# Kernel optimization log

Hardware: AMD Instinct MI355X
Metric: run time of the kernel (lower is better)

The kernel has to match this reference:

```python
import jax, jax.numpy as jnp
import numpy as np

N_HEADS = 16

def setup_inputs() -> dict:
    key = jax.random.key(0)
    ks = jax.random.split(key, 8)
    B, S, D = 2, 2048, 1024
    s = 0.02
    return {
        "hidden_states": jax.random.normal(ks[0], (B, S, D), jnp.float32),
        "attention_mask": jnp.ones((B, S), jnp.int32),
        "script_types": jax.random.randint(ks[1], (B, S), 0, 4),
        "Wq": jax.random.normal(ks[2], (D, D), jnp.float32) * s,
        "bq": jnp.zeros((D,), jnp.float32),
        "Wk": jax.random.normal(ks[3], (D, D), jnp.float32) * s,
        "bk": jnp.zeros((D,), jnp.float32),
        "Wv": jax.random.normal(ks[4], (D, D), jnp.float32) * s,
        "bv": jnp.zeros((D,), jnp.float32),
        "Wo": jax.random.normal(ks[5], (D, D), jnp.float32) * s,
        "bo": jnp.zeros((D,), jnp.float32),
        "script_w": jnp.ones((4, N_HEADS), jnp.float32),
    }

def _heads(x, H):
    B, S, D = x.shape
    return x.reshape(B, S, H, D // H).transpose(0, 2, 1, 3)  # [B,H,S,hd]

def reference(hidden_states, attention_mask, script_types, Wq, bq, Wk, bk, Wv, bv, Wo, bo, script_w):
    B, S, D = hidden_states.shape
    H = N_HEADS
    hd = D // H
    q = _heads(hidden_states @ Wq + bq, H)
    k = _heads(hidden_states @ Wk + bk, H)
    v = _heads(hidden_states @ Wv + bv, H)
    # script-dependent per-head query scaling: [B,S,H] -> [B,H,S,1]
    sw = script_w[script_types].transpose(0, 2, 1)[..., None]
    q = q * sw
    scores = jnp.einsum("bhqd,bhkd->bhqk", q, k) / jnp.sqrt(jnp.float32(hd))
    mask = attention_mask[:, None, None, :]  # [B,1,1,S]
    scores = jnp.where(mask == 0, -jnp.inf, scores)
    probs = jax.nn.softmax(scores, axis=-1)  # dropout is identity in eval mode
    ctx = jnp.einsum("bhqk,bhkd->bhqd", probs, v)
    ctx = ctx.transpose(0, 2, 1, 3).reshape(B, S, D)
    out = ctx @ Wo + bo
    return out, probs
```

## Files before the change

### kernel.cpp

```cpp
#include <hip/hip_runtime.h>
#include <hip/hip_bf16.h>
#include <cstdint>
#include <cstddef>

typedef __attribute__((ext_vector_type(8))) short short8;
typedef __attribute__((ext_vector_type(4))) float f32x4;

#define MFMA16(a,b,c) __builtin_amdgcn_mfma_f32_16x16x32_bf16((a),(b),(c),0,0,0)
#define NEG_INF (-__builtin_inff())

__device__ __forceinline__ unsigned short f2bf(float f) {
    union { float f; unsigned int u; } a; a.f = f;
    return (unsigned short)((a.u + 0x7FFFu + ((a.u >> 16) & 1u)) >> 16);
}

__device__ __forceinline__ unsigned int cvtpk_bf16(float a, float b) {
    unsigned int r;
    asm("v_cvt_pk_bf16_f32 %0, %1, %2" : "=v"(r) : "v"(a), "v"(b));
    return r;
}

__device__ __forceinline__ void gload16(const void* g, void* l) {
    __builtin_amdgcn_global_load_lds(
        (const __attribute__((address_space(1))) void*)g,
        (__attribute__((address_space(3))) void*)l, 16, 0, 0);
}

__global__ __launch_bounds__(256) void prep(const float* __restrict__ X,
                                            unsigned short* __restrict__ Xb,
                                            const float* __restrict__ Wq,
                                            const float* __restrict__ Wk,
                                            const float* __restrict__ Wv,
                                            const float* __restrict__ Wo,
                                            unsigned short* __restrict__ WqkvT,
                                            unsigned short* __restrict__ WoT,
                                            const float* __restrict__ bq,
                                            const float* __restrict__ bk,
                                            const float* __restrict__ bv,
                                            float* __restrict__ biasq) {
    const int bid = blockIdx.x;
    const int t = threadIdx.x;
    if (bid < 4096) {
        int i = (bid * 256 + t) * 4;
        float4 v = *(const float4*)(X + i);
        ushort4 o;
        o.x = f2bf(v.x); o.y = f2bf(v.y); o.z = f2bf(v.z); o.w = f2bf(v.w);
        *(ushort4*)(Xb + i) = o;
    } else if (bid < 8192) {
        __shared__ float tile[32][33];
        const int wid = bid - 4096;
        const int which = wid >> 10, t32 = wid & 1023;
        const float* W = (which == 0) ? Wq : (which == 1) ? Wk : (which == 2) ? Wv : Wo;
        unsigned short* WT = (which < 3) ? (WqkvT + which * 1048576) : WoT;
        int tx = t & 31, ty = t >> 5;
        int kb = (t32 & 31) * 32, nb = (t32 >> 5) * 32;
        #pragma unroll
        for (int r = 0; r < 32; r += 8)
            tile[ty + r][tx] = W[(size_t)(kb + ty + r) * 1024 + nb + tx];
        __syncthreads();
        #pragma unroll
        for (int r = 0; r < 32; r += 8) {
            float v = tile[tx][ty + r];
            WT[(size_t)(nb + ty + r) * 1024 + kb + tx] = f2bf(v);
        }
    } else {
        for (int i = t; i < 3072; i += 256) {
            const float* s = (i < 1024) ? bq : (i < 2048) ? bk : bv;
            biasq[i] = s[i & 1023];
        }
    }
}

__global__ __launch_bounds__(256) void gemm_qkv(const unsigned short* __restrict__ A,
                                                const unsigned short* __restrict__ BT,
                                                const float* __restrict__ bias,
                                                unsigned short* __restrict__ qk_out,
                                                unsigned short* __restrict__ vt_out) {
    __shared__ alignas(16) unsigned short As[4096];
    __shared__ alignas(16) unsigned short Bs[4096];
    const int t = threadIdx.x;
    const int wave = t >> 6, lane = t & 63, quad = lane >> 4, l16 = lane & 15;
    const int m0 = blockIdx.x * 128, n0 = blockIdx.y * 128;
    const int wm = (wave >> 1) * 64, wn = (wave & 1) * 64;
    const int r4 = lane >> 2, c16 = (lane & 3) << 4;
    const char* Ag = (const char*)A + (size_t)(m0 + wave * 32 + r4) * 2048 + c16;
    const char* Bg = (const char*)BT + (size_t)(n0 + wave * 32 + r4) * 2048 + c16;
    char* Al = (char*)As + wave * 2048;
    char* Bl = (char*)Bs + wave * 2048;
    f32x4 acc[4][4] = {};
    for (int k0 = 0; k0 < 1024; k0 += 32) {
        __syncthreads();
        gload16(Ag + k0 * 2, Al);
        gload16(Ag + k0 * 2 + 32768, Al + 1024);
        gload16(Bg + k0 * 2, Bl);
        gload16(Bg + k0 * 2 + 32768, Bl + 1024);
        __syncthreads();
        short8 af[4], bfr[4];
        #pragma unroll
        for (int i = 0; i < 4; i++)
            af[i] = *(const short8*)((const char*)As + (wm + i * 16 + l16) * 64 + (quad << 4));
        #pragma unroll
        for (int j = 0; j < 4; j++)
            bfr[j] = *(const short8*)((const char*)Bs + (wn + j * 16 + l16) * 64 + (quad << 4));
        #pragma unroll
        for (int i = 0; i < 4; i++)
            #pragma unroll
            for (int j = 0; j < 4; j++)
                acc[i][j] = MFMA16(af[i], bfr[j], acc[i][j]);
    }
    #pragma unroll
    for (int i = 0; i < 4; i++) {
        int tokb = m0 + wm + i * 16 + quad * 4;
        int b = tokb >> 11, s = tokb & 2047;
        #pragma unroll
        for (int j = 0; j < 4; j++) {
            int n = n0 + wn + j * 16 + l16;
            float bv = bias[n];
            int which = n >> 10, n1 = n & 1023, h = n1 >> 6, d = n1 & 63;
            if (which == 2) {
                ushort4 pv;
                pv.x = f2bf(acc[i][j][0] + bv);
                pv.y = f2bf(acc[i][j][1] + bv);
                pv.z = f2bf(acc[i][j][2] + bv);
                pv.w = f2bf(acc[i][j][3] + bv);
                *(ushort4*)(vt_out + ((size_t)(b * 16 + h) * 64 + d) * 2048 + s) = pv;
            } else {
                #pragma unroll
                for (int r = 0; r < 4; r++) {
                    float v = acc[i][j][r] + bv;
                    qk_out[(size_t)which * 4194304 +
                           (((size_t)(b * 16 + h)) * 2048 + s + r) * 64 + d] = f2bf(v);
                }
            }
        }
    }
}

__global__ __launch_bounds__(256) void gemm_out(const unsigned short* __restrict__ A,
                                                const unsigned short* __restrict__ BT,
                                                const float* __restrict__ bias,
                                                float* __restrict__ C) {
    __shared__ alignas(16) unsigned short As[2048];
    __shared__ alignas(16) unsigned short Bs[4096];
    const int t = threadIdx.x;
    const int wave = t >> 6, lane = t & 63, quad = lane >> 4, l16 = lane & 15;
    const int m0 = blockIdx.x * 64, n0 = blockIdx.y * 128;
    const int wm = (wave >> 1) * 32, wn = (wave & 1) * 64;
    const int r4 = lane >> 2, c16 = (lane & 3) << 4;
    const char* Ag = (const char*)A + (size_t)(m0 + wave * 16 + r4) * 2048 + c16;
    const char* Bg = (const char*)BT + (size_t)(n0 + wave * 32 + r4) * 2048 + c16;
    char* Al = (char*)As + wave * 1024;
    char* Bl = (char*)Bs + wave * 2048;
    f32x4 acc[2][4] = {};
    for (int k0 = 0; k0 < 1024; k0 += 32) {
        __syncthreads();
        gload16(Ag + k0 * 2, Al);
        gload16(Bg + k0 * 2, Bl);
        gload16(Bg + k0 * 2 + 32768, Bl + 1024);
        __syncthreads();
        short8 af[2], bfr[4];
        #pragma unroll
        for (int i = 0; i < 2; i++)
            af[i] = *(const short8*)((const char*)As + (wm + i * 16 + l16) * 64 + (quad << 4));
        #pragma unroll
        for (int j = 0; j < 4; j++)
            bfr[j] = *(const short8*)((const char*)Bs + (wn + j * 16 + l16) * 64 + (quad << 4));
        #pragma unroll
        for (int i = 0; i < 2; i++)
            #pragma unroll
            for (int j = 0; j < 4; j++)
                acc[i][j] = MFMA16(af[i], bfr[j], acc[i][j]);
    }
    #pragma unroll
    for (int i = 0; i < 2; i++) {
        int tokb = m0 + wm + i * 16 + quad * 4;
        #pragma unroll
        for (int j = 0; j < 4; j++) {
            int n = n0 + wn + j * 16 + l16;
            float bv = bias[n];
            #pragma unroll
            for (int r = 0; r < 4; r++)
                C[(size_t)(tokb + r) * 1024 + n] = acc[i][j][r] + bv;
        }
    }
}

__global__ __launch_bounds__(512, 4) void attn(const unsigned short* __restrict__ Q,
                                               const unsigned short* __restrict__ K,
                                               const unsigned short* __restrict__ Vt,
                                               const int* __restrict__ amask,
                                               const int* __restrict__ stypes,
                                               const float* __restrict__ script_w,
                                               float* __restrict__ probs,
                                               unsigned short* __restrict__ ctx) {
    __shared__ alignas(16) unsigned short KsA[3][4096];
    __shared__ alignas(16) unsigned short VtsA[3][4096];
    __shared__ alignas(16) unsigned short Ps[8][16][64];
    __shared__ alignas(16) float mb[2048];
    const int t = threadIdx.x;
    const int wave = t >> 6, lane = t & 63, quad = lane >> 4, l16 = lane & 15;
    const int bid = blockIdx.y * 16 + blockIdx.x;
    const int swz = (bid & 7) * 64 + (bid >> 3);
    const int qt = swz & 15, bh = swz >> 4;
    const int b = bh >> 4, h = bh & 15;
    const int q0 = qt * 128;
    const int qrow = q0 + wave * 16 + l16;
    const int sx16 = (l16 & 7) << 4;

    const int st = stypes[b * 2048 + qrow];
    const float sfac = script_w[st * 16 + h] * 0.125f;

    const size_t qbase = ((size_t)bh * 2048 + qrow) * 64;
    const short8 aQ0 = *(const short8*)(Q + qbase + quad * 8);
    const short8 aQ1 = *(const short8*)(Q + qbase + 32 + quad * 8);

    const char* Kg = (const char*)(K + (size_t)bh * 131072);
    const char* Vg = (const char*)(Vt + (size_t)bh * 131072);

    {
        int4 m4 = *(const int4*)(amask + b * 2048 + t * 4);
        f32x4 mv;
        mv[0] = m4.x ? 0.f : NEG_INF;
        mv[1] = m4.y ? 0.f : NEG_INF;
        mv[2] = m4.z ? 0.f : NEG_INF;
        mv[3] = m4.w ? 0.f : NEG_INF;
        *(f32x4*)&mb[t * 4] = mv;
    }

    const int r8 = lane >> 3;
    const int cx = ((lane & 7) ^ r8) << 4;
    char* KsB = (char*)&KsA[0][0];
    char* VtsB = (char*)&VtsA[0][0];

#define STAGE_K(kt_, ob_) \
    gload16(Kg + (size_t)(kt_) * 8192 + (wave * 8 + r8) * 128 + cx, KsB + (ob_) + wave * 1024)
#define STAGE_V(kt_, ob_) \
    gload16(Vg + (size_t)(wave * 8 + r8) * 4096 + (kt_) * 128 + cx, VtsB + (ob_) + wave * 1024)
#define QKT(dst_, ob_) do { \
        const char* _kb = KsB + (ob_); \
        _Pragma("unroll") \
        for (int _j = 0; _j < 4; _j++) { \
            const char* _rp = _kb + (_j * 16 + l16) * 128; \
            short8 _k0 = *(const short8*)(_rp + ((quad << 4) ^ sx16)); \
            short8 _k1 = *(const short8*)(_rp + ((64 + (quad << 4)) ^ sx16)); \
            dst_[_j] = MFMA16(_k0, aQ0, dst_[_j]); \
            dst_[_j] = MFMA16(_k1, aQ1, dst_[_j]); \
        } } while (0)

    int ob0 = 0, ob1 = 8192, ob2 = 16384;

    float lsum = 0.f;
    STAGE_K(0, ob0);
    STAGE_K(1, ob1);
    __syncthreads();
    f32x4 sc[4] = {};
    QKT(sc, ob0);
    for (int kt = 0; kt < 32; kt++) {
        if (kt < 30) STAGE_K(kt + 2, ob2);
        #pragma unroll
        for (int j = 0; j < 4; j++) {
            f32x4 mv = *(const f32x4*)&mb[kt * 64 + j * 16 + quad * 4];
            float e0 = __expf(fmaf(sc[j][0], sfac, mv[0]));
            float e1 = __expf(fmaf(sc[j][1], sfac, mv[1]));
            float e2 = __expf(fmaf(sc[j][2], sfac, mv[2]));
            float e3 = __expf(fmaf(sc[j][3], sfac, mv[3]));
            lsum += (e0 + e1) + (e2 + e3);
        }
        f32x4 scn[4] = {};
        if (kt < 31) QKT(scn, ob1);
        __syncthreads();
        int tmp = ob0; ob0 = ob1; ob1 = ob2; ob2 = tmp;
        #pragma unroll
        for (int j = 0; j < 4; j++) sc[j] = scn[j];
    }
    lsum += __shfl_xor(lsum, 16, 64);
    lsum += __shfl_xor(lsum, 32, 64);
    const float inv_l = (lsum > 0.f) ? 1.0f / lsum : 0.0f;

    f32x4 oacc[4] = {};
    ob0 = 0; ob1 = 8192; ob2 = 16384;
    STAGE_K(0, ob0); STAGE_V(0, ob0);
    STAGE_K(1, ob1); STAGE_V(1, ob1);
    __syncthreads();
    f32x4 sc2[4] = {};
    QKT(sc2, ob0);
    char* psrow = (char*)&Ps[wave][l16][0];
    for (int kt = 0; kt < 32; kt++) {
        if (kt < 30) { STAGE_K(kt + 2, ob2); STAGE_V(kt + 2, ob2); }
        const size_t pbase = ((size_t)bh * 2048 + qrow) * 2048 + kt * 64 + quad * 4;
        #pragma unroll
        for (int j = 0; j < 4; j++) {
            f32x4 mv = *(const f32x4*)&mb[kt * 64 + j * 16 + quad * 4];
            float p0 = __expf(fmaf(sc2[j][0], sfac, mv[0])) * inv_l;
            float p1 = __expf(fmaf(sc2[j][1], sfac, mv[1])) * inv_l;
            float p2 = __expf(fmaf(sc2[j][2], sfac, mv[2])) * inv_l;
            float p3 = __expf(fmaf(sc2[j][3], sfac, mv[3])) * inv_l;
            f32x4 pv; pv[0] = p0; pv[1] = p1; pv[2] = p2; pv[3] = p3;
            __builtin_nontemporal_store(pv, (f32x4*)(probs + pbase + j * 16));
            uint2 pq; pq.x = cvtpk_bf16(p0, p1); pq.y = cvtpk_bf16(p2, p3);
            *(uint2*)(psrow + ((j * 32 + quad * 8) ^ sx16)) = pq;
        }
        const char* vbl = VtsB + ob0;
        short8 vv[4];
        #pragma unroll
        for (int j2 = 0; j2 < 4; j2++)
            vv[j2] = *(const short8*)(vbl + (j2 * 16 + l16) * 128 + ((quad << 4) ^ sx16));
        f32x4 scn[4] = {};
        if (kt < 31) QKT(scn, ob1);
        asm volatile("s_waitcnt lgkmcnt(0)" ::: "memory");
        __builtin_amdgcn_sched_barrier(0);
        short8 aP0 = *(const short8*)(psrow + ((quad << 4) ^ sx16));
        short8 aP1 = *(const short8*)(psrow + ((64 + (quad << 4)) ^ sx16));
        __builtin_amdgcn_s_setprio(1);
        #pragma unroll
        for (int j2 = 0; j2 < 4; j2++) oacc[j2] = MFMA16(aP0, vv[j2], oacc[j2]);
        __builtin_amdgcn_s_setprio(0);
        #pragma unroll
        for (int j2 = 0; j2 < 4; j2++)
            vv[j2] = *(const short8*)(vbl + (j2 * 16 + l16) * 128 + ((64 + (quad << 4)) ^ sx16));
        __builtin_amdgcn_s_setprio(1);
        #pragma unroll
        for (int j2 = 0; j2 < 4; j2++) oacc[j2] = MFMA16(aP1, vv[j2], oacc[j2]);
        __builtin_amdgcn_s_setprio(0);
        asm volatile("s_waitcnt vmcnt(4)" ::: "memory");
        __builtin_amdgcn_s_barrier();
        int tmp = ob0; ob0 = ob1; ob1 = ob2; ob2 = tmp;
        #pragma unroll
        for (int j = 0; j < 4; j++) sc2[j] = scn[j];
    }
#undef STAGE_K
#undef STAGE_V
#undef QKT
    #pragma unroll
    for (int j2 = 0; j2 < 4; j2++)
        #pragma unroll
        for (int r = 0; r < 4; r++) {
            int qr = q0 + wave * 16 + quad * 4 + r;
            ctx[((size_t)b * 2048 + qr) * 1024 + h * 64 + j2 * 16 + l16] = f2bf(oacc[j2][r]);
        }
}

extern "C" void kernel_launch(void* const* d_in, const int* in_sizes, int n_in,
                              void* d_out, int out_size, void* d_ws, size_t ws_size,
                              hipStream_t stream) {
    const float* X    = (const float*)d_in[0];
    const int*  amask = (const int*)d_in[1];
    const int*  stp   = (const int*)d_in[2];
    const float* Wq   = (const float*)d_in[3];
    const float* bq   = (const float*)d_in[4];
    const float* Wk   = (const float*)d_in[5];
    const float* bk   = (const float*)d_in[6];
    const float* Wv   = (const float*)d_in[7];
    const float* bv   = (const float*)d_in[8];
    const float* Wo   = (const float*)d_in[9];
    const float* bo   = (const float*)d_in[10];
    const float* sw   = (const float*)d_in[11];

    float* out   = (float*)d_out;
    float* probs = out + 4194304;

    char* ws = (char*)d_ws;
    unsigned short* Xb    = (unsigned short*)(ws);
    unsigned short* WqkvT = (unsigned short*)(ws + 8388608);
    unsigned short* WoT   = (unsigned short*)(ws + 14680064);
    float*          biasq = (float*)(ws + 16777216);
    unsigned short* Qb    = (unsigned short*)(ws + 16789504);
    unsigned short* Vtb   = (unsigned short*)(ws + 41955328);
    unsigned short* Ctx   = (unsigned short*)(ws + 50343936);
    unsigned short* Kb    = Qb + 4194304;

    prep<<<8193, 256, 0, stream>>>(X, Xb, Wq, Wk, Wv, Wo, WqkvT, WoT, bq, bk, bv, biasq);
    gemm_qkv<<<dim3(32, 24), 256, 0, stream>>>(Xb, WqkvT, biasq, Qb, Vtb);
    attn<<<dim3(16, 32), 512, 0, stream>>>(Qb, Kb, Vtb, amask, stp, sw, probs, Ctx);
    gemm_out<<<dim3(64, 8), 256, 0, stream>>>(Ctx, WoT, bo, out);
}
```

Before: 288.2 us.

## Split attention into row-sum kernel and probs/context kernel

Moves the first pass, which computes softmax denominators, into its own kernel. That kernel uses less shared memory and allows higher occupancy (launch bounds 6), and it writes the inverse row sums to workspace. The second kernel reads those sums and does the probability write and the PV product. This lets the light first pass run at higher occupancy and frees the heavy kernel from carrying the first loop. The cost is an extra kernel launch and an extra global round trip for the row sums.

```diff
diff --git a/kernel.cpp b/kernel.cpp
--- a/kernel.cpp
+++ b/kernel.cpp
@@ -185,14 +185,103 @@
     }
 }
 
-__global__ __launch_bounds__(512, 4) void attn(const unsigned short* __restrict__ Q,
-                                               const unsigned short* __restrict__ K,
-                                               const unsigned short* __restrict__ Vt,
-                                               const int* __restrict__ amask,
-                                               const int* __restrict__ stypes,
-                                               const float* __restrict__ script_w,
-                                               float* __restrict__ probs,
-                                               unsigned short* __restrict__ ctx) {
+__global__ __launch_bounds__(512, 6) void attn_p1(const unsigned short* __restrict__ Q,
+                                                  const unsigned short* __restrict__ K,
+                                                  const int* __restrict__ amask,
+                                                  const int* __restrict__ stypes,
+                                                  const float* __restrict__ script_w,
+                                                  float* __restrict__ invl) {
+    __shared__ alignas(16) unsigned short KsA[3][4096];
+    __shared__ alignas(16) float mb[2048];
+    const int t = threadIdx.x;
+    const int wave = t >> 6, lane = t & 63, quad = lane >> 4, l16 = lane & 15;
+    const int bid = blockIdx.y * 16 + blockIdx.x;
+    const int swz = (bid & 7) * 64 + (bid >> 3);
+    const int qt = swz & 15, bh = swz >> 4;
+    const int b = bh >> 4, h = bh & 15;
+    const int q0 = qt * 128;
+    const int qrow = q0 + wave * 16 + l16;
+    const int sx16 = (l16 & 7) << 4;
+
+    const int st = stypes[b * 2048 + qrow];
+    const float sfac = script_w[st * 16 + h] * 0.125f;
+
+    const size_t qbase = ((size_t)bh * 2048 + qrow) * 64;
+    const short8 aQ0 = *(const short8*)(Q + qbase + quad * 8);
+    const short8 aQ1 = *(const short8*)(Q + qbase + 32 + quad * 8);
+
+    const char* Kg = (const char*)(K + (size_t)bh * 131072);
+
+    {
+        int4 m4 = *(const int4*)(amask + b * 2048 + t * 4);
+        f32x4 mv;
+        mv[0] = m4.x ? 0.f : NEG_INF;
+        mv[1] = m4.y ? 0.f : NEG_INF;
+        mv[2] = m4.z ? 0.f : NEG_INF;
+        mv[3] = m4.w ? 0.f : NEG_INF;
+        *(f32x4*)&mb[t * 4] = mv;
+    }
+
+    const int r8 = lane >> 3;
+    const int cx = ((lane & 7) ^ r8) << 4;
+    char* KsB = (char*)&KsA[0][0];
+
+#define STAGE_K1(kt_, ob_) \
+    gload16(Kg + (size_t)(kt_) * 8192 + (wave * 8 + r8) * 128 + cx, KsB + (ob_) + wave * 1024)
+#define QKT1(dst_, ob_) do { \
+        const char* _kb = KsB + (ob_); \
+        _Pragma("unroll") \
+        for (int _j = 0; _j < 4; _j++) { \
+            const char* _rp = _kb + (_j * 16 + l16) * 128; \
+            short8 _k0 = *(const short8*)(_rp + ((quad << 4) ^ sx16)); \
+            short8 _k1 = *(const short8*)(_rp + ((64 + (quad << 4)) ^ sx16)); \
+            dst_[_j] = MFMA16(_k0, aQ0, dst_[_j]); \
+            dst_[_j] = MFMA16(_k1, aQ1, dst_[_j]); \
+        } } while (0)
+
+    int ob0 = 0, ob1 = 8192, ob2 = 16384;
+    float lsum = 0.f;
+    STAGE_K1(0, ob0);
+    STAGE_K1(1, ob1);
+    __syncthreads();
+    f32x4 sc[4] = {};
+    QKT1(sc, ob0);
+    for (int kt = 0; kt < 32; kt++) {
+        if (kt < 30) STAGE_K1(kt + 2, ob2);
+        #pragma unroll
+        for (int j = 0; j < 4; j++) {
+            f32x4 mv = *(const f32x4*)&mb[kt * 64 + j * 16 + quad * 4];
+            float e0 = __expf(fmaf(sc[j][0], sfac, mv[0]));
+            float e1 = __expf(fmaf(sc[j][1], sfac, mv[1]));
+            float e2 = __expf(fmaf(sc[j][2], sfac, mv[2]));
+            float e3 = __expf(fmaf(sc[j][3], sfac, mv[3]));
+            lsum += (e0 + e1) + (e2 + e3);
+        }
+        f32x4 scn[4] = {};
+        if (kt < 31) QKT1(scn, ob1);
+        __syncthreads();
+        int tmp = ob0; ob0 = ob1; ob1 = ob2; ob2 = tmp;
+        #pragma unroll
+        for (int j = 0; j < 4; j++) sc[j] = scn[j];
+    }
+#undef STAGE_K1
+#undef QKT1
+    lsum += __shfl_xor(lsum, 16, 64);
+    lsum += __shfl_xor(lsum, 32, 64);
+    const float inv_l = (lsum > 0.f) ? 1.0f / lsum : 0.0f;
+    if (lane < 16)
+        invl[(size_t)bh * 2048 + q0 + wave * 16 + lane] = inv_l;
+}
+
+__global__ __launch_bounds__(512, 4) void attn_p2(const unsigned short* __restrict__ Q,
+                                                  const unsigned short* __restrict__ K,
+                                                  const unsigned short* __restrict__ Vt,
+                                                  const int* __restrict__ amask,
+                                                  const int* __restrict__ stypes,
+                                                  const float* __restrict__ script_w,
+                                                  const float* __restrict__ invl,
+                                                  float* __restrict__ probs,
+                                                  unsigned short* __restrict__ ctx) {
     __shared__ alignas(16) unsigned short KsA[3][4096];
     __shared__ alignas(16) unsigned short VtsA[3][4096];
     __shared__ alignas(16) unsigned short Ps[8][16][64];
@@ -209,6 +298,7 @@
 
     const int st = stypes[b * 2048 + qrow];
     const float sfac = script_w[st * 16 + h] * 0.125f;
+    const float inv_l = invl[(size_t)bh * 2048 + qrow];
 
     const size_t qbase = ((size_t)bh * 2048 + qrow) * 64;
     const short8 aQ0 = *(const short8*)(Q + qbase + quad * 8);
@@ -232,11 +322,11 @@
     char* KsB = (char*)&KsA[0][0];
     char* VtsB = (char*)&VtsA[0][0];
 
-#define STAGE_K(kt_, ob_) \
+#define STAGE_K2(kt_, ob_) \
     gload16(Kg + (size_t)(kt_) * 8192 + (wave * 8 + r8) * 128 + cx, KsB + (ob_) + wave * 1024)
-#define STAGE_V(kt_, ob_) \
+#define STAGE_V2(kt_, ob_) \
     gload16(Vg + (size_t)(wave * 8 + r8) * 4096 + (kt_) * 128 + cx, VtsB + (ob_) + wave * 1024)
-#define QKT(dst_, ob_) do { \
+#define QKT2(dst_, ob_) do { \
         const char* _kb = KsB + (ob_); \
         _Pragma("unroll") \
         for (int _j = 0; _j < 4; _j++) { \
@@ -248,45 +338,15 @@
         } } while (0)
 
     int ob0 = 0, ob1 = 8192, ob2 = 16384;
-
-    float lsum = 0.f;
-    STAGE_K(0, ob0);
-    STAGE_K(1, ob1);
-    __syncthreads();
-    f32x4 sc[4] = {};
-    QKT(sc, ob0);
-    for (int kt = 0; kt < 32; kt++) {
-        if (kt < 30) STAGE_K(kt + 2, ob2);
-        #pragma unroll
-        for (int j = 0; j < 4; j++) {
-            f32x4 mv = *(const f32x4*)&mb[kt * 64 + j * 16 + quad * 4];
-            float e0 = __expf(fmaf(sc[j][0], sfac, mv[0]));
-            float e1 = __expf(fmaf(sc[j][1], sfac, mv[1]));
-            float e2 = __expf(fmaf(sc[j][2], sfac, mv[2]));
-            float e3 = __expf(fmaf(sc[j][3], sfac, mv[3]));
-            lsum += (e0 + e1) + (e2 + e3);
-        }
-        f32x4 scn[4] = {};
-        if (kt < 31) QKT(scn, ob1);
-        __syncthreads();
-        int tmp = ob0; ob0 = ob1; ob1 = ob2; ob2 = tmp;
-        #pragma unroll
-        for (int j = 0; j < 4; j++) sc[j] = scn[j];
-    }
-    lsum += __shfl_xor(lsum, 16, 64);
-    lsum += __shfl_xor(lsum, 32, 64);
-    const float inv_l = (lsum > 0.f) ? 1.0f / lsum : 0.0f;
-
     f32x4 oacc[4] = {};
-    ob0 = 0; ob1 = 8192; ob2 = 16384;
-    STAGE_K(0, ob0); STAGE_V(0, ob0);
-    STAGE_K(1, ob1); STAGE_V(1, ob1);
+    STAGE_K2(0, ob0); STAGE_V2(0, ob0);
+    STAGE_K2(1, ob1); STAGE_V2(1, ob1);
     __syncthreads();
     f32x4 sc2[4] = {};
-    QKT(sc2, ob0);
+    QKT2(sc2, ob0);
     char* psrow = (char*)&Ps[wave][l16][0];
     for (int kt = 0; kt < 32; kt++) {
-        if (kt < 30) { STAGE_K(kt + 2, ob2); STAGE_V(kt + 2, ob2); }
+        if (kt < 30) { STAGE_K2(kt + 2, ob2); STAGE_V2(kt + 2, ob2); }
         const size_t pbase = ((size_t)bh * 2048 + qrow) * 2048 + kt * 64 + quad * 4;
         #pragma unroll
         for (int j = 0; j < 4; j++) {
@@ -306,7 +366,7 @@
         for (int j2 = 0; j2 < 4; j2++)
             vv[j2] = *(const short8*)(vbl + (j2 * 16 + l16) * 128 + ((quad << 4) ^ sx16));
         f32x4 scn[4] = {};
-        if (kt < 31) QKT(scn, ob1);
+        if (kt < 31) QKT2(scn, ob1);
         asm volatile("s_waitcnt lgkmcnt(0)" ::: "memory");
         __builtin_amdgcn_sched_barrier(0);
         short8 aP0 = *(const short8*)(psrow + ((quad << 4) ^ sx16));
@@ -328,9 +388,9 @@
         #pragma unroll
         for (int j = 0; j < 4; j++) sc2[j] = scn[j];
     }
-#undef STAGE_K
-#undef STAGE_V
-#undef QKT
+#undef STAGE_K2
+#undef STAGE_V2
+#undef QKT2
     #pragma unroll
     for (int j2 = 0; j2 < 4; j2++)
         #pragma unroll
@@ -365,12 +425,14 @@
     unsigned short* WoT   = (unsigned short*)(ws + 14680064);
     float*          biasq = (float*)(ws + 16777216);
     unsigned short* Qb    = (unsigned short*)(ws + 16789504);
+    float*          invl  = (float*)(ws + 33566720);
     unsigned short* Vtb   = (unsigned short*)(ws + 41955328);
     unsigned short* Ctx   = (unsigned short*)(ws + 50343936);
     unsigned short* Kb    = Qb + 4194304;
 
     prep<<<8193, 256, 0, stream>>>(X, Xb, Wq, Wk, Wv, Wo, WqkvT, WoT, bq, bk, bv, biasq);
     gemm_qkv<<<dim3(32, 24), 256, 0, stream>>>(Xb, WqkvT, biasq, Qb, Vtb);
-    attn<<<dim3(16, 32), 512, 0, stream>>>(Qb, Kb, Vtb, amask, stp, sw, probs, Ctx);
+    attn_p1<<<dim3(16, 32), 512, 0, stream>>>(Qb, Kb, amask, stp, sw, invl);
+    attn_p2<<<dim3(16, 32), 512, 0, stream>>>(Qb, Kb, Vtb, amask, stp, sw, invl, probs, Ctx);
     gemm_out<<<dim3(64, 8), 256, 0, stream>>>(Ctx, WoT, bo, out);
 }
```

Measured after the change: 299.1 us. 1.04x slower.
